# Kernel tuning notes

Measured on AMD Instinct MI355X. Metric: run time of the kernel, lower is better.

Reference implementation:

```python
import jax, jax.numpy as jnp
import numpy as np

K, PMAX, NUM_PTS = 20000, 30, 5
GEO_DIM, PE_DIM = 256, 32
C_OUT = GEO_DIM - PE_DIM  # 224
NUM_FREQS = 8


def setup_inputs() -> dict:
    key = jax.random.key(0)
    k = jax.random.split(key, 6)
    geoms = jax.random.normal(k[0], (K, PMAX, 2), dtype=jnp.float32) * 8.0  # ego BEV meters
    lengths = jax.random.randint(k[1], (K,), 2, PMAX + 1)                   # valid points per polyline
    w1 = jax.random.normal(k[2], (C_OUT // 2, 2, 3), jnp.float32) * 0.2
    b1 = jax.random.normal(k[3], (C_OUT // 2,), jnp.float32) * 0.02
    w2 = jax.random.normal(k[4], (C_OUT, C_OUT // 2, 3), jnp.float32) * 0.05
    b2 = jax.random.normal(k[5], (C_OUT,), jnp.float32) * 0.02
    gamma = jnp.ones((C_OUT,), jnp.float32)
    beta = jnp.zeros((C_OUT,), jnp.float32)
    return {"geoms": geoms, "lengths": lengths, "w1": w1, "b1": b1,
            "w2": w2, "b2": b2, "gamma": gamma, "beta": beta,
            "roi_w": 60, "roi_h": 30}


def _resample_one(coords, L):
    # coords: [PMAX,2] padded polyline; L: scalar int (>=2 valid points)
    diffs = coords[1:] - coords[:-1]                                  # [PMAX-1,2]
    sq = jnp.sum(diffs * diffs, axis=1)
    mask = (jnp.arange(PMAX - 1) < (L - 1)).astype(coords.dtype)      # valid segments
    seg = jnp.where(sq > 0, jnp.sqrt(jnp.where(sq > 0, sq, 1.0)), 0.0) * mask
    cum = jnp.concatenate([jnp.zeros((1,), coords.dtype), jnp.cumsum(seg)])  # [PMAX]
    total = cum[-1]
    targets = jnp.linspace(0.0, 1.0, NUM_PTS, dtype=coords.dtype) * total
    idx = jnp.clip(jnp.searchsorted(cum, targets, side='left'), 1, L - 1)
    t = (targets - cum[idx - 1]) / (seg[idx - 1] + 1e-8)
    pts = coords[idx - 1] + t[:, None] * diffs[idx - 1]               # [NUM_PTS,2]
    degen = total < 1e-6
    return jnp.where(degen, jnp.broadcast_to(coords[0], pts.shape), pts)


def _conv1d(x, w, b):
    # x: [K,C,5]; w: [O,C,3]; 'same' padding 1
    y = jax.lax.conv_general_dilated(x, w, (1,), ((1, 1),),
                                     dimension_numbers=('NCH', 'OIH', 'NCH'))
    return y + b[None, :, None]


def reference(geoms, lengths, w1, b1, w2, b2, gamma, beta, roi_w, roi_h):
    resampled = jax.vmap(_resample_one)(geoms, lengths)               # [K,5,2]
    roi_half = jnp.array([roi_w / 2.0, roi_h / 2.0], jnp.float32)
    roi_full = jnp.array([float(roi_w), float(roi_h)], jnp.float32)
    coords = (resampled + roi_half) / roi_full                        # [K,5,2] in [0,1]
    # sinusoidal PE: per coord dim [sin(x*2^f*pi) x8 | cos x8] -> flatten to 32
    freqs = (2.0 ** jnp.arange(NUM_FREQS, dtype=jnp.float32)) * np.float32(np.pi)
    xf = coords[..., None] * freqs                                    # [K,5,2,8]
    pe = jnp.concatenate([jnp.sin(xf), jnp.cos(xf)], axis=-1).reshape(-1, NUM_PTS, PE_DIM)
    x = coords.transpose(0, 2, 1)                                     # [K,2,5]
    x = jax.nn.relu(_conv1d(x, w1, b1))                               # [K,112,5]
    x = jax.nn.relu(_conv1d(x, w2, b2))                               # [K,224,5]
    x = x.transpose(0, 2, 1)                                          # [K,5,224]
    mu = jnp.mean(x, axis=-1, keepdims=True)
    var = jnp.mean((x - mu) ** 2, axis=-1, keepdims=True)
    x = (x - mu) * jax.lax.rsqrt(var + 1e-5) * gamma + beta
    geo_feats = jnp.concatenate([pe, x], axis=-1)                     # [K,5,256]
    return geo_feats, coords
```

## Files before the change

kernel.cpp:

```cpp
#include <hip/hip_runtime.h>
#include <math.h>

#define K_POLY   20000
#define PMAX     30
#define NUM_PTS  5
#define C_MID    112
#define C_OUT    224
#define PE_DIM   32
#define GEO_DIM  256
#define M_ROWS   (K_POLY*NUM_PTS)

#define NTILES   14
#define KSTEPS   11
#define WP_ELEMS (KSTEPS*NTILES*64*8)
#define NPACK_BLK ((WP_ELEMS+255)/256)
#define POLY_PER_BLK 4
#define NPREP_BLK ((K_POLY+POLY_PER_BLK-1)/POLY_PER_BLK)

#define CHUNK_STRIDE 2560
#define CHUNK_OFF    64

#define ROWS_W   30
#define NUNITS   ((M_ROWS+ROWS_W-1)/ROWS_W)
#define WAVES2_B 8
#define NBLK2    256
#define TOTW2    (NBLK2*WAVES2_B)

typedef __attribute__((ext_vector_type(8))) short short8;
typedef __attribute__((ext_vector_type(4))) float f32x4;

__device__ inline unsigned short f2bf(float f) {
    union { float f; unsigned u; } v; v.f = f;
    return (unsigned short)((v.u + 0x7fffu + ((v.u >> 16) & 1u)) >> 16);
}

#define GLDS(gp, lp) __builtin_amdgcn_global_load_lds( \
    (const __attribute__((address_space(1))) void*)(gp), \
    (__attribute__((address_space(3))) void*)(lp), 16, 0, 0)

__global__ __launch_bounds__(256) void prep_pack(
    const float* __restrict__ geoms, const int* __restrict__ lengths,
    const float* __restrict__ w1, const float* __restrict__ b1,
    const float* __restrict__ w2,
    const int* __restrict__ roi_w, const int* __restrict__ roi_h,
    unsigned short* __restrict__ Wp, float* __restrict__ out)
{
    if (blockIdx.x < NPACK_BLK) {
        int i = blockIdx.x * 256 + threadIdx.x;
        if (i < WP_ELEMS) {
            int j    = i & 7;
            int lane = (i >> 3) & 63;
            int grp  = i >> 9;
            int nt   = grp % NTILES;
            int ks   = grp / NTILES;
            int k    = ks * 32 + (lane >> 4) * 8 + j;
            int n    = nt * 16 + (lane & 15);
            float v = 0.f;
            if (k < 336) {
                int dk = k / C_MID, c = k - dk * C_MID;
                v = w2[(n * C_MID + c) * 3 + dk];
            }
            Wp[i] = f2bf(v);
        }
        return;
    }

    const int poly = (blockIdx.x - NPACK_BLK) * POLY_PER_BLK + (threadIdx.x >> 6);
    const int lane = threadIdx.x & 63;
    if (poly >= K_POLY) return;

    const float* gp = geoms + (size_t)poly * (PMAX * 2);
    float px = 0.f, py = 0.f;
    if (lane < PMAX) { float2 p = ((const float2*)gp)[lane]; px = p.x; py = p.y; }
    const int L = lengths[poly];

    float nx = __shfl(px, lane + 1);
    float ny = __shfl(py, lane + 1);
    float seg = 0.f;
    if (lane < L - 1 && lane < PMAX - 1) {
        float dx = nx - px, dy = ny - py;
        float sq = dx * dx + dy * dy;
        seg = (sq > 0.f) ? sqrtf(sq) : 0.f;
    }
    float incl = seg;
    #pragma unroll
    for (int d = 1; d < 32; d <<= 1) {
        float v = __shfl_up(incl, d, 32);
        if ((lane & 31) >= d) incl += v;
    }
    float cum = __shfl_up(incl, 1, 32);
    if ((lane & 31) == 0) cum = 0.f;
    const float total = __shfl(incl, PMAX - 2);

    const float roiw = (float)roi_w[0], roih = (float)roi_h[0];
    const float halfx = roiw * 0.5f, halfy = roih * 0.5f;
    const bool degen = total < 1e-6f;
    const float x0g = __shfl(px, 0), y0g = __shfl(py, 0);

    float bxv[NUM_PTS], byv[NUM_PTS];
    #pragma unroll
    for (int j = 0; j < NUM_PTS; ++j) {
        float tj = total * (0.25f * (float)j);
        unsigned long long mlt = __ballot(lane < PMAX && cum < tj);
        int idx = (int)__popcll(mlt);
        idx = max(1, min(idx, L - 1));
        float c1 = __shfl(cum, idx - 1);
        float s1 = __shfl(seg, idx - 1);
        float ax = __shfl(px, idx - 1), ay = __shfl(py, idx - 1);
        float bx2 = __shfl(px, idx),    by2 = __shfl(py, idx);
        float tt = (tj - c1) / (s1 + 1e-8f);
        float fx = degen ? x0g : ax + tt * (bx2 - ax);
        float fy = degen ? y0g : ay + tt * (by2 - ay);
        bxv[j] = (fx + halfx) / roiw;
        byv[j] = (fy + halfy) / roih;
    }
    if (lane == 0) {
        float* co = out + (size_t)M_ROWS * GEO_DIM + (size_t)poly * (NUM_PTS * 2);
        #pragma unroll
        for (int j = 0; j < NUM_PTS; ++j) { co[2 * j] = bxv[j]; co[2 * j + 1] = byv[j]; }
    }

    unsigned short* chunk = (unsigned short*)out + (size_t)poly * CHUNK_STRIDE + CHUNK_OFF;
    unsigned int* cz = (unsigned int*)chunk;
    if (lane < 56) cz[lane] = 0u;
    cz[336 + lane] = 0u;

    #pragma unroll
    for (int it = 0; it < 2; ++it) {
        int c = it * 64 + lane;
        if (c < C_MID) {
            const float* w = w1 + c * 6;
            float w0 = w[0], wa = w[1], wb = w[2], w3 = w[3], w4 = w[4], w5 = w[5];
            float bb = b1[c];
            #pragma unroll
            for (int p = 0; p < NUM_PTS; ++p) {
                float acc = bb + bxv[p] * wa + byv[p] * w4;
                if (p > 0)           acc += bxv[p - 1] * w0 + byv[p - 1] * w3;
                if (p < NUM_PTS - 1) acc += bxv[p + 1] * wb + byv[p + 1] * w5;
                chunk[(p + 1) * C_MID + c] = f2bf(fmaxf(acc, 0.f));
            }
        }
    }
}

__global__ __launch_bounds__(512, 2) void gemm2(
    const unsigned short* __restrict__ Wp,
    const float* __restrict__ b2, const float* __restrict__ gamma,
    const float* __restrict__ beta, float* __restrict__ out)
{
    __shared__ __align__(16) unsigned short s_B[WP_ELEMS];

    const int t = threadIdx.x, lane = t & 63, wave = t >> 6;
    const int quad = lane >> 4, m = lane & 15;

    #pragma unroll
    for (int it = 0; it < 20; ++it) {
        int idx = t + it * 512;
        if (idx < WP_ELEMS / 8)
            GLDS((const char*)Wp + (size_t)idx * 16, (char*)s_B + idx * 16);
    }
    __syncthreads();

    const unsigned short* A = (const unsigned short*)out;
    const float* cptr = out + (size_t)M_ROWS * GEO_DIM;
    const unsigned short* bl = s_B + lane * 8;

    for (int u = blockIdx.x * WAVES2_B + wave; u < NUNITS; u += TOTW2) {
        const int rw = u * ROWS_W;

        int r0 = min(rw + m, M_ROWS - 1);
        int r1 = min(rw + 16 + m, M_ROWS - 1);
        int poly0 = r0 / 5, p0 = r0 - poly0 * 5;
        int poly1 = r1 / 5, p1 = r1 - poly1 * 5;
        const unsigned short* Ab0 = A + (size_t)poly0 * CHUNK_STRIDE + CHUNK_OFF + p0 * C_MID + quad * 8;
        const unsigned short* Ab1 = A + (size_t)poly1 * CHUNK_STRIDE + CHUNK_OFF + p1 * C_MID + quad * 8;

        f32x4 acc0[NTILES], acc1[NTILES];
        #pragma unroll
        for (int nt = 0; nt < NTILES; ++nt)
            #pragma unroll
            for (int i = 0; i < 4; ++i) { acc0[nt][i] = 0.f; acc1[nt][i] = 0.f; }

        short8 a0 = *(const short8*)Ab0;
        short8 a1 = *(const short8*)Ab1;
        #pragma unroll
        for (int ks = 0; ks < KSTEPS; ++ks) {
            short8 a0n = a0, a1n = a1;
            if (ks < KSTEPS - 1) {
                a0n = *(const short8*)(Ab0 + (ks + 1) * 32);
                a1n = *(const short8*)(Ab1 + (ks + 1) * 32);
            }
            const unsigned short* bp = bl + ks * (NTILES * 512);
            __builtin_amdgcn_s_setprio(1);
            #pragma unroll
            for (int nt = 0; nt < NTILES; ++nt) {
                short8 b = *(const short8*)(bp + nt * 512);
                acc0[nt] = __builtin_amdgcn_mfma_f32_16x16x32_bf16(a0, b, acc0[nt], 0, 0, 0);
                acc1[nt] = __builtin_amdgcn_mfma_f32_16x16x32_bf16(a1, b, acc1[nt], 0, 0, 0);
            }
            __builtin_amdgcn_s_setprio(0);
            a0 = a0n; a1 = a1n;
        }

        {
            const int col = lane & 31;
            const int d = col >> 4, isc = (col >> 3) & 1, fr = col & 7;
            const float pef = (float)(1 << fr) * 3.14159265358979323846f;
            #pragma unroll
            for (int it = 0; it < 15; ++it) {
                int r = rw + it * 2 + (lane >> 5);
                if (r < M_ROWS) {
                    float x = cptr[(size_t)r * 2 + d];
                    float arg = x * pef;
                    out[(size_t)r * GEO_DIM + col] = isc ? __cosf(arg) : __sinf(arg);
                }
            }
        }

        float bias[NTILES], gm[NTILES], bt[NTILES];
        #pragma unroll
        for (int nt = 0; nt < NTILES; ++nt) {
            int col = nt * 16 + m;
            bias[nt] = b2[col]; gm[nt] = gamma[col]; bt[nt] = beta[col];
        }

        #pragma unroll
        for (int g = 0; g < 2; ++g) {
            f32x4* acc = g ? acc1 : acc0;
            #pragma unroll
            for (int i = 0; i < 4; ++i) {
                float s = 0.f, q = 0.f;
                #pragma unroll
                for (int nt = 0; nt < NTILES; ++nt) {
                    float v = fmaxf(acc[nt][i] + bias[nt], 0.f);
                    acc[nt][i] = v;
                    s += v; q += v * v;
                }
                #pragma unroll
                for (int mk = 8; mk >= 1; mk >>= 1) {
                    s += __shfl_xor(s, mk, 64);
                    q += __shfl_xor(q, mk, 64);
                }
                float mu  = s * (1.f / C_OUT);
                float var = fmaxf(q * (1.f / C_OUT) - mu * mu, 0.f);
                float rs  = rsqrtf(var + 1e-5f);
                int r = rw + g * 16 + quad * 4 + i;
                if (r < M_ROWS && !(g == 1 && quad == 3 && i >= 2)) {
                    size_t ob = (size_t)r * GEO_DIM + PE_DIM + m;
                    #pragma unroll
                    for (int nt = 0; nt < NTILES; ++nt)
                        out[ob + nt * 16] = (acc[nt][i] - mu) * rs * gm[nt] + bt[nt];
                }
            }
        }
    }
}

extern "C" void kernel_launch(void* const* d_in, const int* in_sizes, int n_in,
                              void* d_out, int out_size, void* d_ws, size_t ws_size,
                              hipStream_t stream) {
    const float* geoms   = (const float*)d_in[0];
    const int*   lengths = (const int*)d_in[1];
    const float* w1      = (const float*)d_in[2];
    const float* b1      = (const float*)d_in[3];
    const float* w2      = (const float*)d_in[4];
    const float* b2      = (const float*)d_in[5];
    const float* gamma   = (const float*)d_in[6];
    const float* beta    = (const float*)d_in[7];
    const int*   roi_w   = (const int*)d_in[8];
    const int*   roi_h   = (const int*)d_in[9];
    float* out = (float*)d_out;
    unsigned short* Wp = (unsigned short*)d_ws;

    hipLaunchKernelGGL(prep_pack, dim3(NPACK_BLK + NPREP_BLK), dim3(256), 0, stream,
                       geoms, lengths, w1, b1, w2, roi_w, roi_h, Wp, out);
    hipLaunchKernelGGL(gemm2, dim3(NBLK2), dim3(512), 0, stream, Wp, b2, gamma, beta, out);
}
```

Measured before the change: 166.3 us.

## Store conv1 activations in MFMA fragment layout and enlarge gemm2 blocks

The prep kernel now writes the im2col'd conv1 output directly in the MFMA A-fragment order (16-row groups, 512-element k-slices), with each activation replicated into its three tap positions. gemm2 can then load its A fragments with contiguous per-lane reads instead of gathered per-row loads. gemm2 also moves to 32-row units with 12 waves per block, loads coords once per unit via shuffle, and caches bias/gamma/beta in LDS. The cost is three times the activation writes in prep, scattered stores in fragment order, and a scratch region inside the output buffer that gemm2 overwrites, which risks a race between units reading and writing it.

```diff
diff --git a/kernel.cpp b/kernel.cpp
--- a/kernel.cpp
+++ b/kernel.cpp
@@ -17,12 +17,11 @@
 #define POLY_PER_BLK 4
 #define NPREP_BLK ((K_POLY+POLY_PER_BLK-1)/POLY_PER_BLK)
 
-#define CHUNK_STRIDE 2560
-#define CHUNK_OFF    64
-
-#define ROWS_W   30
-#define NUNITS   ((M_ROWS+ROWS_W-1)/ROWS_W)
-#define WAVES2_B 8
+#define GROUP_US 8192
+
+#define ROWS_W   32
+#define NUNITS   (M_ROWS/ROWS_W)
+#define WAVES2_B 12
 #define NBLK2    256
 #define TOTW2    (NBLK2*WAVES2_B)
 
@@ -37,6 +36,12 @@
 #define GLDS(gp, lp) __builtin_amdgcn_global_load_lds( \
     (const __attribute__((address_space(1))) void*)(gp), \
     (__attribute__((address_space(3))) void*)(lp), 16, 0, 0)
+
+__device__ inline void store_frag(unsigned short* Af, int r, int k, unsigned short v) {
+    size_t addr = (size_t)(r >> 4) * GROUP_US + (size_t)(k >> 5) * 512
+                + (size_t)(((((k >> 3) & 3) << 4) + (r & 15)) << 3) + (k & 7);
+    Af[addr] = v;
+}
 
 __global__ __launch_bounds__(256) void prep_pack(
     const float* __restrict__ geoms, const int* __restrict__ lengths,
@@ -120,10 +125,11 @@
         for (int j = 0; j < NUM_PTS; ++j) { co[2 * j] = bxv[j]; co[2 * j + 1] = byv[j]; }
     }
 
-    unsigned short* chunk = (unsigned short*)out + (size_t)poly * CHUNK_STRIDE + CHUNK_OFF;
-    unsigned int* cz = (unsigned int*)chunk;
-    if (lane < 56) cz[lane] = 0u;
-    cz[336 + lane] = 0u;
+    unsigned short* Af = (unsigned short*)out;
+    const int rbase = poly * NUM_PTS;
+
+    for (int z = lane; z < 80; z += 64)
+        store_frag(Af, rbase + (z >> 4), 336 + (z & 15), 0);
 
     #pragma unroll
     for (int it = 0; it < 2; ++it) {
@@ -132,48 +138,60 @@
             const float* w = w1 + c * 6;
             float w0 = w[0], wa = w[1], wb = w[2], w3 = w[3], w4 = w[4], w5 = w[5];
             float bb = b1[c];
-            #pragma unroll
-            for (int p = 0; p < NUM_PTS; ++p) {
-                float acc = bb + bxv[p] * wa + byv[p] * w4;
-                if (p > 0)           acc += bxv[p - 1] * w0 + byv[p - 1] * w3;
-                if (p < NUM_PTS - 1) acc += bxv[p + 1] * wb + byv[p + 1] * w5;
-                chunk[(p + 1) * C_MID + c] = f2bf(fmaxf(acc, 0.f));
-            }
-        }
-    }
-}
-
-__global__ __launch_bounds__(512, 2) void gemm2(
+            store_frag(Af, rbase + 0, c, 0);
+            store_frag(Af, rbase + 4, 224 + c, 0);
+            #pragma unroll
+            for (int pp = 0; pp < NUM_PTS; ++pp) {
+                float acc = bb + bxv[pp] * wa + byv[pp] * w4;
+                if (pp > 0)           acc += bxv[pp - 1] * w0 + byv[pp - 1] * w3;
+                if (pp < NUM_PTS - 1) acc += bxv[pp + 1] * wb + byv[pp + 1] * w5;
+                unsigned short hv = f2bf(fmaxf(acc, 0.f));
+                #pragma unroll
+                for (int dk = 0; dk < 3; ++dk) {
+                    int p = pp + 1 - dk;
+                    if (p >= 0 && p < NUM_PTS)
+                        store_frag(Af, rbase + p, dk * C_MID + c, hv);
+                }
+            }
+        }
+    }
+}
+
+__global__ __launch_bounds__(768, 3) void gemm2(
     const unsigned short* __restrict__ Wp,
     const float* __restrict__ b2, const float* __restrict__ gamma,
     const float* __restrict__ beta, float* __restrict__ out)
 {
     __shared__ __align__(16) unsigned short s_B[WP_ELEMS];
+    __shared__ float s_ln[3 * C_OUT];
 
     const int t = threadIdx.x, lane = t & 63, wave = t >> 6;
     const int quad = lane >> 4, m = lane & 15;
 
     #pragma unroll
-    for (int it = 0; it < 20; ++it) {
-        int idx = t + it * 512;
+    for (int it = 0; it < 13; ++it) {
+        int idx = t + it * 768;
         if (idx < WP_ELEMS / 8)
             GLDS((const char*)Wp + (size_t)idx * 16, (char*)s_B + idx * 16);
     }
+    if (t < C_OUT) {
+        s_ln[t]             = b2[t];
+        s_ln[C_OUT + t]     = gamma[t];
+        s_ln[2 * C_OUT + t] = beta[t];
+    }
     __syncthreads();
 
-    const unsigned short* A = (const unsigned short*)out;
+    const unsigned short* Af = (const unsigned short*)out;
     const float* cptr = out + (size_t)M_ROWS * GEO_DIM;
     const unsigned short* bl = s_B + lane * 8;
 
     for (int u = blockIdx.x * WAVES2_B + wave; u < NUNITS; u += TOTW2) {
         const int rw = u * ROWS_W;
 
-        int r0 = min(rw + m, M_ROWS - 1);
-        int r1 = min(rw + 16 + m, M_ROWS - 1);
-        int poly0 = r0 / 5, p0 = r0 - poly0 * 5;
-        int poly1 = r1 / 5, p1 = r1 - poly1 * 5;
-        const unsigned short* Ab0 = A + (size_t)poly0 * CHUNK_STRIDE + CHUNK_OFF + p0 * C_MID + quad * 8;
-        const unsigned short* Ab1 = A + (size_t)poly1 * CHUNK_STRIDE + CHUNK_OFF + p1 * C_MID + quad * 8;
+        const unsigned short* Ab0 = Af + (size_t)(2 * u) * GROUP_US + lane * 8;
+        const unsigned short* Ab1 = Ab0 + GROUP_US;
+
+        float cv = cptr[(size_t)rw * 2 + lane];
 
         f32x4 acc0[NTILES], acc1[NTILES];
         #pragma unroll
@@ -187,8 +205,8 @@
         for (int ks = 0; ks < KSTEPS; ++ks) {
             short8 a0n = a0, a1n = a1;
             if (ks < KSTEPS - 1) {
-                a0n = *(const short8*)(Ab0 + (ks + 1) * 32);
-                a1n = *(const short8*)(Ab1 + (ks + 1) * 32);
+                a0n = *(const short8*)(Ab0 + (ks + 1) * 512);
+                a1n = *(const short8*)(Ab1 + (ks + 1) * 512);
             }
             const unsigned short* bp = bl + ks * (NTILES * 512);
             __builtin_amdgcn_s_setprio(1);
@@ -207,21 +225,23 @@
             const int d = col >> 4, isc = (col >> 3) & 1, fr = col & 7;
             const float pef = (float)(1 << fr) * 3.14159265358979323846f;
             #pragma unroll
-            for (int it = 0; it < 15; ++it) {
-                int r = rw + it * 2 + (lane >> 5);
-                if (r < M_ROWS) {
-                    float x = cptr[(size_t)r * 2 + d];
-                    float arg = x * pef;
-                    out[(size_t)r * GEO_DIM + col] = isc ? __cosf(arg) : __sinf(arg);
-                }
-            }
-        }
-
+            for (int it = 0; it < 16; ++it) {
+                int j2 = it * 2 + (lane >> 5);
+                float x = __shfl(cv, j2 * 2 + d);
+                float arg = x * pef;
+                out[(size_t)(rw + j2) * GEO_DIM + col] = isc ? __cosf(arg) : __sinf(arg);
+            }
+        }
+
+        unsigned lnoff = 0;
+        asm volatile("" : "+v"(lnoff));
         float bias[NTILES], gm[NTILES], bt[NTILES];
         #pragma unroll
         for (int nt = 0; nt < NTILES; ++nt) {
-            int col = nt * 16 + m;
-            bias[nt] = b2[col]; gm[nt] = gamma[col]; bt[nt] = beta[col];
+            unsigned col = lnoff + nt * 16 + m;
+            bias[nt] = s_ln[col];
+            gm[nt]   = s_ln[C_OUT + col];
+            bt[nt]   = s_ln[2 * C_OUT + col];
         }
 
         #pragma unroll
@@ -245,12 +265,10 @@
                 float var = fmaxf(q * (1.f / C_OUT) - mu * mu, 0.f);
                 float rs  = rsqrtf(var + 1e-5f);
                 int r = rw + g * 16 + quad * 4 + i;
-                if (r < M_ROWS && !(g == 1 && quad == 3 && i >= 2)) {
-                    size_t ob = (size_t)r * GEO_DIM + PE_DIM + m;
-                    #pragma unroll
-                    for (int nt = 0; nt < NTILES; ++nt)
-                        out[ob + nt * 16] = (acc[nt][i] - mu) * rs * gm[nt] + bt[nt];
-                }
+                size_t ob = (size_t)r * GEO_DIM + PE_DIM + m;
+                #pragma unroll
+                for (int nt = 0; nt < NTILES; ++nt)
+                    out[ob + nt * 16] = (acc[nt][i] - mu) * rs * gm[nt] + bt[nt];
             }
         }
     }
@@ -274,5 +292,5 @@
 
     hipLaunchKernelGGL(prep_pack, dim3(NPACK_BLK + NPREP_BLK), dim3(256), 0, stream,
                        geoms, lengths, w1, b1, w2, roi_w, roi_h, Wp, out);
-    hipLaunchKernelGGL(gemm2, dim3(NBLK2), dim3(512), 0, stream, Wp, b2, gamma, beta, out);
-}
+    hipLaunchKernelGGL(gemm2, dim3(NBLK2), dim3(768), 0, stream, Wp, b2, gamma, beta, out);
+}
```

Result: slower. 193.2 us (+16.2%).
